# Kernel tuning notes

Hardware: AMD Instinct MI355X
Metric: run time of the kernel (lower is better)

## Reference

```python
import jax, jax.numpy as jnp
import numpy as np

N = 100000
E = 600000
H = 128
L = 2  # mp_ngcn


def setup_inputs() -> dict:
    key = jax.random.key(0)
    k = jax.random.split(key, 8)
    h = jax.random.normal(k[0], (N, H), dtype=jnp.float32)
    edge_row = jax.random.randint(k[1], (E,), 0, N, dtype=jnp.int32)
    edge_col = jax.random.randint(k[2], (E,), 0, N, dtype=jnp.int32)
    edge_w = jax.random.uniform(k[3], (E,), dtype=jnp.float32)
    # xavier_normal gain=1.414 for square fc: std = 1.414*sqrt(2/(H+H))
    std = 1.414 * np.sqrt(2.0 / (H + H))
    fc_w = jax.random.normal(k[4], (L, H, H), dtype=jnp.float32) * std
    fc_b = jnp.zeros((L, H), dtype=jnp.float32)           # init 0.0
    gcn_bias = jnp.full((L, H), 0.001, dtype=jnp.float32)  # init 0.001
    prelu_a = jnp.full((L,), 0.25, dtype=jnp.float32)      # PReLU default
    return {"h": h, "edge_row": edge_row, "edge_col": edge_col,
            "edge_w": edge_w, "fc_w": fc_w, "fc_b": fc_b,
            "gcn_bias": gcn_bias, "prelu_a": prelu_a}


def reference(h, edge_row, edge_col, edge_w, fc_w, fc_b, gcn_bias, prelu_a):
    x = h
    for i in range(L):
        # dense linear transform: [N,H] @ [H,H]^T + b
        s = x @ fc_w[i].T + fc_b[i]
        # sparse adjacency spmm: out[r] = sum_e w_e * s[c_e]
        msg = s[edge_col] * edge_w[:, None]        # [E,H] gather + scale
        out = jax.ops.segment_sum(msg, edge_row, num_segments=N)
        out = out + gcn_bias[i]
        # dropout (eval-mode identity), then PReLU
        x = jnp.where(out > 0, out, prelu_a[i] * out)
    return x
```

## Files before the change

kernel.cpp:

```cpp
#include <hip/hip_runtime.h>

#define H 128
#define ELLW 64
#define CPAD 16

typedef __attribute__((ext_vector_type(8))) short bf16x8;
typedef __attribute__((ext_vector_type(4))) short s16x4;
typedef __attribute__((ext_vector_type(4))) float f32x4;

__device__ inline unsigned short f2bf(float f) {
    unsigned u = __float_as_uint(f);
    unsigned r = (u + 0x7fffu + ((u >> 16) & 1u)) >> 16;
    return (unsigned short)r;
}
__device__ inline float bflo(unsigned u) { return __uint_as_float(u << 16); }
__device__ inline float bfhi(unsigned u) { return __uint_as_float(u & 0xffff0000u); }

__device__ inline unsigned pack_cw(int c, float w) {
    unsigned q = (unsigned)(w * 32768.f);
    if (q > 32767u) q = 32767u;
    return ((unsigned)c << 15) | q;
}

#define MB 64

template<bool BF16IN>
__global__ __launch_bounds__(256) void gemm_mfma_kernel(
    const void* __restrict__ xv, const float* __restrict__ W,
    const float* __restrict__ b, short* __restrict__ s_out, int N, int nbatch)
{
    __shared__ short wlds[H * 136];

    const int t = threadIdx.x;
    const int l = t & 63;
    const int w = t >> 6;
    const int n_g   = (w & 1) * 32;
    const int col_g = (w >> 1) * 64;
    const int ln15 = l & 15;
    const int lhi  = l >> 4;

    #pragma unroll
    for (int i = 0; i < 16; ++i) {
        int fidx = i * 256 + t;
        int j  = fidx >> 5;
        int c4 = fidx & 31;
        float4 v = *reinterpret_cast<const float4*>(W + (size_t)j * H + c4 * 4);
        s16x4 p;
        p[0] = (short)f2bf(v.x); p[1] = (short)f2bf(v.y);
        p[2] = (short)f2bf(v.z); p[3] = (short)f2bf(v.w);
        *reinterpret_cast<s16x4*>(&wlds[j * 136 + c4 * 4]) = p;
    }

    float4 bias4[4];
    #pragma unroll
    for (int jt = 0; jt < 4; ++jt)
        bias4[jt] = *reinterpret_cast<const float4*>(b + col_g + jt * 16 + lhi * 4);

    __syncthreads();

    for (int batch = blockIdx.x; batch < nbatch; batch += gridDim.x) {
        const int row0 = batch * MB;

        bf16x8 ax[4][2];
        #pragma unroll
        for (int nf = 0; nf < 2; ++nf) {
            const int n = row0 + n_g + nf * 16 + ln15;
            const bool ok = (n < N);
            #pragma unroll
            for (int ks = 0; ks < 4; ++ks) {
                bf16x8 f = {0, 0, 0, 0, 0, 0, 0, 0};
                if (ok) {
                    if (BF16IN) {
                        f = *reinterpret_cast<const bf16x8*>(
                            (const short*)xv + (size_t)n * H + ks * 32 + lhi * 8);
                    } else {
                        const float* p = (const float*)xv + (size_t)n * H + ks * 32 + lhi * 8;
                        float4 lo = *reinterpret_cast<const float4*>(p);
                        float4 hi = *reinterpret_cast<const float4*>(p + 4);
                        f[0] = (short)f2bf(lo.x); f[1] = (short)f2bf(lo.y);
                        f[2] = (short)f2bf(lo.z); f[3] = (short)f2bf(lo.w);
                        f[4] = (short)f2bf(hi.x); f[5] = (short)f2bf(hi.y);
                        f[6] = (short)f2bf(hi.z); f[7] = (short)f2bf(hi.w);
                    }
                }
                ax[ks][nf] = f;
            }
        }

        f32x4 acc[2][4] = {};
        #pragma unroll
        for (int ks = 0; ks < 4; ++ks) {
            #pragma unroll
            for (int jt = 0; jt < 4; ++jt) {
                bf16x8 aw = *reinterpret_cast<const bf16x8*>(
                    &wlds[(col_g + jt * 16 + ln15) * 136 + ks * 32 + lhi * 8]);
                acc[0][jt] = __builtin_amdgcn_mfma_f32_16x16x32_bf16(
                    aw, ax[ks][0], acc[0][jt], 0, 0, 0);
                acc[1][jt] = __builtin_amdgcn_mfma_f32_16x16x32_bf16(
                    aw, ax[ks][1], acc[1][jt], 0, 0, 0);
            }
        }

        #pragma unroll
        for (int nf = 0; nf < 2; ++nf) {
            const int n = row0 + n_g + nf * 16 + ln15;
            if (n < N) {
                #pragma unroll
                for (int jt = 0; jt < 4; ++jt) {
                    s16x4 p;
                    p[0] = (short)f2bf(acc[nf][jt][0] + bias4[jt].x);
                    p[1] = (short)f2bf(acc[nf][jt][1] + bias4[jt].y);
                    p[2] = (short)f2bf(acc[nf][jt][2] + bias4[jt].z);
                    p[3] = (short)f2bf(acc[nf][jt][3] + bias4[jt].w);
                    *reinterpret_cast<s16x4*>(
                        s_out + (size_t)n * H + col_g + jt * 16 + lhi * 4) = p;
                }
            }
        }
    }
}

__global__ __launch_bounds__(256) void zero_kernel(int4* __restrict__ p, int n4)
{
    int i = blockIdx.x * blockDim.x + threadIdx.x;
    const int stride = gridDim.x * blockDim.x;
    for (; i < n4; i += stride) p[i] = make_int4(0, 0, 0, 0);
}

__global__ __launch_bounds__(256) void count_fill_kernel(
    const int* __restrict__ erow, const int* __restrict__ ecol,
    const float* __restrict__ ew, int* __restrict__ counts,
    unsigned* __restrict__ cw, int E)
{
    int e = blockIdx.x * blockDim.x + threadIdx.x;
    if (e < E) {
        int r = erow[e];
        int rk = atomicAdd(&counts[(size_t)r * CPAD], 1);
        if (rk < ELLW)
            cw[(size_t)r * ELLW + rk] = pack_cw(ecol[e], ew[e]);
    }
}

template<int MODE>
__global__ __launch_bounds__(256) void spmm_ell8_kernel(
    const int* __restrict__ counts, const unsigned* __restrict__ cw,
    const short* __restrict__ s_bf, const float* __restrict__ gbias,
    const float* __restrict__ a_ptr, float* __restrict__ out_f,
    short* __restrict__ out_b, int N)
{
    const float a = a_ptr[0];
    int gid = blockIdx.x * blockDim.x + threadIdx.x;
    int wid  = gid >> 6;
    int l    = gid & 63;
    int half = l >> 5;
    int li   = l & 31;
    int r = wid * 2 + half;
    if (r >= N) return;

    int cnt = counts[(size_t)r * CPAD];
    if (cnt > ELLW) cnt = ELLW;
    const unsigned* __restrict__ base = cw + (size_t)r * ELLW;
    const size_t coff = (size_t)li * 4;
    const float SC = 1.f / 32768.f;

    float ac0[4] = {0.f, 0.f, 0.f, 0.f};
    float ac1[4] = {0.f, 0.f, 0.f, 0.f};
    float ac2[4] = {0.f, 0.f, 0.f, 0.f};
    float ac3[4] = {0.f, 0.f, 0.f, 0.f};

    for (int e0 = 0; e0 < cnt; e0 += 8) {
        unsigned p[8];
        #pragma unroll
        for (int k = 0; k < 8; ++k) {
            unsigned pk = base[e0 + k];
            p[k] = (e0 + k < cnt) ? pk : 0u;
        }
        unsigned long long u[8];
        #pragma unroll
        for (int k = 0; k < 8; ++k)
            u[k] = *reinterpret_cast<const unsigned long long*>(
                s_bf + (size_t)(p[k] >> 15) * H + coff);
        #pragma unroll
        for (int k = 0; k < 8; ++k) {
            float wk = (float)(p[k] & 0x7fffu) * SC;
            unsigned lo = (unsigned)u[k];
            unsigned hi = (unsigned)(u[k] >> 32);
            float* ac = (k & 3) == 0 ? ac0 : (k & 3) == 1 ? ac1
                       : (k & 3) == 2 ? ac2 : ac3;
            ac[0] += wk * bflo(lo); ac[1] += wk * bfhi(lo);
            ac[2] += wk * bflo(hi); ac[3] += wk * bfhi(hi);
        }
    }

    float4 g = *reinterpret_cast<const float4*>(gbias + li * 4);
    float v0 = (ac0[0] + ac1[0]) + (ac2[0] + ac3[0]) + g.x;
    float v1 = (ac0[1] + ac1[1]) + (ac2[1] + ac3[1]) + g.y;
    float v2 = (ac0[2] + ac1[2]) + (ac2[2] + ac3[2]) + g.z;
    float v3 = (ac0[3] + ac1[3]) + (ac2[3] + ac3[3]) + g.w;
    v0 = v0 > 0.f ? v0 : a * v0;
    v1 = v1 > 0.f ? v1 : a * v1;
    v2 = v2 > 0.f ? v2 : a * v2;
    v3 = v3 > 0.f ? v3 : a * v3;

    if (MODE == 0) {
        *reinterpret_cast<float4*>(out_f + (size_t)r * H + li * 4) =
            make_float4(v0, v1, v2, v3);
    } else {
        s16x4 p;
        p[0] = (short)f2bf(v0); p[1] = (short)f2bf(v1);
        p[2] = (short)f2bf(v2); p[3] = (short)f2bf(v3);
        *reinterpret_cast<s16x4*>(out_b + (size_t)r * H + li * 4) = p;
    }
}

__global__ __launch_bounds__(256) void init_out_kernel(
    float* __restrict__ out, const float* __restrict__ gbias, int total4)
{
    int i = blockIdx.x * blockDim.x + threadIdx.x;
    const int stride = gridDim.x * blockDim.x;
    for (; i < total4; i += stride) {
        int c4 = i & 31;
        float4 bv = *reinterpret_cast<const float4*>(gbias + c4 * 4);
        *reinterpret_cast<float4*>(out + (size_t)i * 4) = bv;
    }
}

__global__ __launch_bounds__(256) void spmm_edge_kernel(
    const int* __restrict__ erow, const int* __restrict__ ecol,
    const float* __restrict__ ew, const short* __restrict__ s_bf,
    float* __restrict__ out, int E)
{
    long long gid = (long long)blockIdx.x * blockDim.x + threadIdx.x;
    int e = (int)(gid >> 6);
    int l = (int)(gid & 63);
    if (e >= E) return;
    int r = erow[e];
    int c = ecol[e];
    float w = ew[e];
    unsigned u = *reinterpret_cast<const unsigned*>(s_bf + (size_t)c * H + 2 * l);
    unsafeAtomicAdd(out + (size_t)r * H + l * 2 + 0, bflo(u) * w);
    unsafeAtomicAdd(out + (size_t)r * H + l * 2 + 1, bfhi(u) * w);
}

__global__ __launch_bounds__(256) void prelu_kernel(
    float* __restrict__ buf, const float* __restrict__ a_ptr, int total4)
{
    const float a = a_ptr[0];
    int i = blockIdx.x * blockDim.x + threadIdx.x;
    const int stride = gridDim.x * blockDim.x;
    for (; i < total4; i += stride) {
        float4 v = *reinterpret_cast<float4*>(buf + (size_t)i * 4);
        v.x = v.x > 0.f ? v.x : a * v.x;
        v.y = v.y > 0.f ? v.y : a * v.y;
        v.z = v.z > 0.f ? v.z : a * v.z;
        v.w = v.w > 0.f ? v.w : a * v.w;
        *reinterpret_cast<float4*>(buf + (size_t)i * 4) = v;
    }
}

extern "C" void kernel_launch(void* const* d_in, const int* in_sizes, int n_in,
                              void* d_out, int out_size, void* d_ws, size_t ws_size,
                              hipStream_t stream)
{
    const float* h        = (const float*)d_in[0];
    const int*   erow     = (const int*)d_in[1];
    const int*   ecol     = (const int*)d_in[2];
    const float* ew       = (const float*)d_in[3];
    const float* fc_w     = (const float*)d_in[4];
    const float* fc_b     = (const float*)d_in[5];
    const float* gcn_bias = (const float*)d_in[6];
    const float* prelu_a  = (const float*)d_in[7];

    const int N = in_sizes[0] / H;
    const int E = in_sizes[1];
    float* out = (float*)d_out;

    char* ws = (char*)d_ws;
    short* s_bf  = (short*)ws;
    size_t off = (size_t)N * H * sizeof(short);
    short* x1_bf = (short*)(ws + off); off += (size_t)N * H * sizeof(short);
    off = (off + 63) & ~(size_t)63;
    int* counts  = (int*)(ws + off); off += (size_t)N * CPAD * 4;
    off = (off + 63) & ~(size_t)63;
    unsigned* cw = (unsigned*)(ws + off); off += (size_t)N * ELLW * 4;

    const int eblocks = (E + 255) / 256;
    const int nbatch = (N + MB - 1) / MB;
    const int ggrid = nbatch < 1024 ? nbatch : 1024;

    if (off <= ws_size) {
        const int n4 = N * CPAD / 4;
        zero_kernel<<<2048, 256, 0, stream>>>((int4*)counts, n4);
        count_fill_kernel<<<eblocks, 256, 0, stream>>>(erow, ecol, ew, counts, cw, E);

        const int spmm_blocks = (int)((((long long)(N + 1) / 2) * 64 + 255) / 256);

        gemm_mfma_kernel<false><<<ggrid, 256, 0, stream>>>(h, fc_w, fc_b, s_bf, N, nbatch);
        spmm_ell8_kernel<1><<<spmm_blocks, 256, 0, stream>>>(
            counts, cw, s_bf, gcn_bias, prelu_a, nullptr, x1_bf, N);
        gemm_mfma_kernel<true><<<ggrid, 256, 0, stream>>>(
            x1_bf, fc_w + H * H, fc_b + H, s_bf, N, nbatch);
        spmm_ell8_kernel<0><<<spmm_blocks, 256, 0, stream>>>(
            counts, cw, s_bf, gcn_bias + H, prelu_a + 1, out, nullptr, N);
    } else {
        const int total4 = N * (H / 4);
        const int spmm_blocks = (int)(((long long)E * 64 + 255) / 256);

        gemm_mfma_kernel<false><<<ggrid, 256, 0, stream>>>(h, fc_w, fc_b, s_bf, N, nbatch);
        init_out_kernel<<<2048, 256, 0, stream>>>(out, gcn_bias, total4);
        spmm_edge_kernel<<<spmm_blocks, 256, 0, stream>>>(erow, ecol, ew, s_bf, out, E);
        prelu_kernel<<<2048, 256, 0, stream>>>(out, prelu_a, total4);

        gemm_mfma_kernel<false><<<ggrid, 256, 0, stream>>>(out, fc_w + H * H, fc_b + H, s_bf, N, nbatch);
        init_out_kernel<<<2048, 256, 0, stream>>>(out, gcn_bias + H, total4);
        spmm_edge_kernel<<<spmm_blocks, 256, 0, stream>>>(erow, ecol, ew, s_bf, out, E);
        prelu_kernel<<<2048, 256, 0, stream>>>(out, prelu_a + 1, total4);
    }
}
```

Before: 143.4 us.

## Fuse ELL build with first GEMM and use sentinel-terminated ELL rows

Merges the edge-to-ELL construction and the first dense GEMM into one launch, splitting the grid into dedicated build blocks and GEMM blocks so the atomic scatter overlaps the MFMA work. Column indices are stored offset by one so a zeroed slot acts as a terminator, which lets the SpMM drop its per-row count read and stop on a zero sentinel. The zero pass now clears the whole ELL array (much larger than the count array), adding memory traffic. Rows are no longer bounded by their count, so one extra group of padding slots may be loaded per row.

```diff
diff --git a/kernel.cpp b/kernel.cpp
--- a/kernel.cpp
+++ b/kernel.cpp
@@ -3,6 +3,7 @@
 #define H 128
 #define ELLW 64
 #define CPAD 16
+#define BUILD_BLOCKS 256
 
 typedef __attribute__((ext_vector_type(8))) short bf16x8;
 typedef __attribute__((ext_vector_type(4))) short s16x4;
@@ -19,18 +20,17 @@
 __device__ inline unsigned pack_cw(int c, float w) {
     unsigned q = (unsigned)(w * 32768.f);
     if (q > 32767u) q = 32767u;
-    return ((unsigned)c << 15) | q;
+    return ((unsigned)(c + 1) << 15) | q;
 }
 
 #define MB 64
 
 template<bool BF16IN>
-__global__ __launch_bounds__(256) void gemm_mfma_kernel(
-    const void* __restrict__ xv, const float* __restrict__ W,
-    const float* __restrict__ b, short* __restrict__ s_out, int N, int nbatch)
-{
-    __shared__ short wlds[H * 136];
-
+__device__ __forceinline__ void gemm_body(
+    short* wlds, const void* __restrict__ xv, const float* __restrict__ W,
+    const float* __restrict__ b, short* __restrict__ s_out, int N, int nbatch,
+    int bid, int grid)
+{
     const int t = threadIdx.x;
     const int l = t & 63;
     const int w = t >> 6;
@@ -58,7 +58,7 @@
 
     __syncthreads();
 
-    for (int batch = blockIdx.x; batch < nbatch; batch += gridDim.x) {
+    for (int batch = bid; batch < nbatch; batch += grid) {
         const int row0 = batch * MB;
 
         bf16x8 ax[4][2];
@@ -120,6 +120,37 @@
     }
 }
 
+template<bool BF16IN>
+__global__ __launch_bounds__(256) void gemm_mfma_kernel(
+    const void* __restrict__ xv, const float* __restrict__ W,
+    const float* __restrict__ b, short* __restrict__ s_out, int N, int nbatch)
+{
+    __shared__ short wlds[H * 136];
+    gemm_body<BF16IN>(wlds, xv, W, b, s_out, N, nbatch, blockIdx.x, gridDim.x);
+}
+
+__global__ __launch_bounds__(256) void build_plus_gemm_kernel(
+    const int* __restrict__ erow, const int* __restrict__ ecol,
+    const float* __restrict__ ew, int* __restrict__ counts,
+    unsigned* __restrict__ cw, int E,
+    const float* __restrict__ h, const float* __restrict__ W0,
+    const float* __restrict__ b0, short* __restrict__ s_bf, int N, int nbatch)
+{
+    __shared__ short wlds[H * 136];
+    if ((int)blockIdx.x < BUILD_BLOCKS) {
+        const int stride = BUILD_BLOCKS * 256;
+        for (int e = blockIdx.x * 256 + threadIdx.x; e < E; e += stride) {
+            int r = erow[e];
+            int rk = atomicAdd(&counts[(size_t)r * CPAD], 1);
+            if (rk < ELLW)
+                cw[(size_t)r * ELLW + rk] = pack_cw(ecol[e], ew[e]);
+        }
+        return;
+    }
+    gemm_body<false>(wlds, h, W0, b0, s_bf, N, nbatch,
+                     (int)blockIdx.x - BUILD_BLOCKS, gridDim.x - BUILD_BLOCKS);
+}
+
 __global__ __launch_bounds__(256) void zero_kernel(int4* __restrict__ p, int n4)
 {
     int i = blockIdx.x * blockDim.x + threadIdx.x;
@@ -127,26 +158,11 @@
     for (; i < n4; i += stride) p[i] = make_int4(0, 0, 0, 0);
 }
 
-__global__ __launch_bounds__(256) void count_fill_kernel(
-    const int* __restrict__ erow, const int* __restrict__ ecol,
-    const float* __restrict__ ew, int* __restrict__ counts,
-    unsigned* __restrict__ cw, int E)
-{
-    int e = blockIdx.x * blockDim.x + threadIdx.x;
-    if (e < E) {
-        int r = erow[e];
-        int rk = atomicAdd(&counts[(size_t)r * CPAD], 1);
-        if (rk < ELLW)
-            cw[(size_t)r * ELLW + rk] = pack_cw(ecol[e], ew[e]);
-    }
-}
-
 template<int MODE>
-__global__ __launch_bounds__(256) void spmm_ell8_kernel(
-    const int* __restrict__ counts, const unsigned* __restrict__ cw,
-    const short* __restrict__ s_bf, const float* __restrict__ gbias,
-    const float* __restrict__ a_ptr, float* __restrict__ out_f,
-    short* __restrict__ out_b, int N)
+__global__ __launch_bounds__(256) void spmm_ellst_kernel(
+    const unsigned* __restrict__ cw, const short* __restrict__ s_bf,
+    const float* __restrict__ gbias, const float* __restrict__ a_ptr,
+    float* __restrict__ out_f, short* __restrict__ out_b, int N)
 {
     const float a = a_ptr[0];
     int gid = blockIdx.x * blockDim.x + threadIdx.x;
@@ -157,8 +173,6 @@
     int r = wid * 2 + half;
     if (r >= N) return;
 
-    int cnt = counts[(size_t)r * CPAD];
-    if (cnt > ELLW) cnt = ELLW;
     const unsigned* __restrict__ base = cw + (size_t)r * ELLW;
     const size_t coff = (size_t)li * 4;
     const float SC = 1.f / 32768.f;
@@ -168,18 +182,18 @@
     float ac2[4] = {0.f, 0.f, 0.f, 0.f};
     float ac3[4] = {0.f, 0.f, 0.f, 0.f};
 
-    for (int e0 = 0; e0 < cnt; e0 += 8) {
+    for (int e0 = 0; e0 < ELLW; e0 += 8) {
         unsigned p[8];
         #pragma unroll
+        for (int k = 0; k < 8; ++k) p[k] = base[e0 + k];
+        unsigned long long u[8];
+        #pragma unroll
         for (int k = 0; k < 8; ++k) {
-            unsigned pk = base[e0 + k];
-            p[k] = (e0 + k < cnt) ? pk : 0u;
-        }
-        unsigned long long u[8];
-        #pragma unroll
-        for (int k = 0; k < 8; ++k)
+            int c = (int)(p[k] >> 15) - 1;
+            c = c < 0 ? 0 : c;
             u[k] = *reinterpret_cast<const unsigned long long*>(
-                s_bf + (size_t)(p[k] >> 15) * H + coff);
+                s_bf + (size_t)c * H + coff);
+        }
         #pragma unroll
         for (int k = 0; k < 8; ++k) {
             float wk = (float)(p[k] & 0x7fffu) * SC;
@@ -190,6 +204,7 @@
             ac[0] += wk * bflo(lo); ac[1] += wk * bfhi(lo);
             ac[2] += wk * bflo(hi); ac[3] += wk * bfhi(hi);
         }
+        if (p[7] == 0u) break;
     }
 
     float4 g = *reinterpret_cast<const float4*>(gbias + li * 4);
@@ -280,28 +295,30 @@
     size_t off = (size_t)N * H * sizeof(short);
     short* x1_bf = (short*)(ws + off); off += (size_t)N * H * sizeof(short);
     off = (off + 63) & ~(size_t)63;
+    size_t zero_beg = off;
     int* counts  = (int*)(ws + off); off += (size_t)N * CPAD * 4;
-    off = (off + 63) & ~(size_t)63;
     unsigned* cw = (unsigned*)(ws + off); off += (size_t)N * ELLW * 4;
-
-    const int eblocks = (E + 255) / 256;
+    size_t zero_end = off;
+
     const int nbatch = (N + MB - 1) / MB;
     const int ggrid = nbatch < 1024 ? nbatch : 1024;
+    const int g0grid = nbatch < 768 ? nbatch : 768;
 
     if (off <= ws_size) {
-        const int n4 = N * CPAD / 4;
-        zero_kernel<<<2048, 256, 0, stream>>>((int4*)counts, n4);
-        count_fill_kernel<<<eblocks, 256, 0, stream>>>(erow, ecol, ew, counts, cw, E);
+        const int n4 = (int)((zero_end - zero_beg) / 16);
+        zero_kernel<<<2048, 256, 0, stream>>>((int4*)(ws + zero_beg), n4);
+        build_plus_gemm_kernel<<<BUILD_BLOCKS + g0grid, 256, 0, stream>>>(
+            erow, ecol, ew, counts, cw, E,
+            h, fc_w, fc_b, s_bf, N, nbatch);
 
         const int spmm_blocks = (int)((((long long)(N + 1) / 2) * 64 + 255) / 256);
 
-        gemm_mfma_kernel<false><<<ggrid, 256, 0, stream>>>(h, fc_w, fc_b, s_bf, N, nbatch);
-        spmm_ell8_kernel<1><<<spmm_blocks, 256, 0, stream>>>(
-            counts, cw, s_bf, gcn_bias, prelu_a, nullptr, x1_bf, N);
+        spmm_ellst_kernel<1><<<spmm_blocks, 256, 0, stream>>>(
+            cw, s_bf, gcn_bias, prelu_a, nullptr, x1_bf, N);
         gemm_mfma_kernel<true><<<ggrid, 256, 0, stream>>>(
             x1_bf, fc_w + H * H, fc_b + H, s_bf, N, nbatch);
-        spmm_ell8_kernel<0><<<spmm_blocks, 256, 0, stream>>>(
-            counts, cw, s_bf, gcn_bias + H, prelu_a + 1, out, nullptr, N);
+        spmm_ellst_kernel<0><<<spmm_blocks, 256, 0, stream>>>(
+            cw, s_bf, gcn_bias + H, prelu_a + 1, out, nullptr, N);
     } else {
         const int total4 = N * (H / 4);
         const int spmm_blocks = (int)(((long long)E * 64 + 255) / 256);
```

Measured after the change: 133.5 us (median of 2 runs). -6.9%, faster.
